# Optimization experiments

Hardware: AMD Instinct MI355X
Metric: run time of the kernel (lower is better)

The kernel has to match this reference:

```python
import jax, jax.numpy as jnp
import numpy as np

DIM = 96
WS = 16            # window_size
OVERLAP = 0.5
UPSCALE = 2
NH = 1             # num_heads
OWIN = int(WS * OVERLAP) + WS          # 24, overlap_win_size
WSU = UPSCALE * WS                     # 32, window_size_up
TABLE = (WSU + OWIN - 1) ** 2          # 3025
PAD = (OWIN - WS) // 2                 # 4


def compute_rpi():
    # Faithful to calculate_rpi_owxra (incl. torch negative-index wraparound -> modulo).
    wsu, cur = WSU, WS + int(OVERLAP * WS)
    a = np.arange(wsu)
    coords_up = np.stack(np.meshgrid(a, a, indexing='ij')).reshape(2, -1)      # (2, wsu^2)
    b = np.arange(cur)
    coords_cur = np.stack(np.meshgrid(b, b, indexing='ij')).reshape(2, -1)     # (2, cur^2)
    rel = coords_cur[:, None, :] - coords_up[:, :, None]                       # (2, wsu^2, cur^2)
    rel = rel.transpose(1, 2, 0).astype(np.int64)
    rel += wsu - cur + 1
    rel[:, :, 0] *= wsu + cur - 1
    idx = rel.sum(-1) % TABLE                                                  # (wsu^2, cur^2)
    return jnp.asarray(idx)


def setup_inputs() -> dict:
    key = jax.random.key(0)
    ks = jax.random.split(key, 6)
    x = jax.random.normal(ks[0], (2, 128, 128, DIM), dtype=jnp.float32)
    x2 = jax.random.normal(ks[1], (128, WSU * WSU, DIM), dtype=jnp.float32)  # (b*nw, 1024, 96)
    Wkv = jax.random.normal(ks[2], (DIM, 2 * DIM), dtype=jnp.float32) * 0.02
    bkv = jnp.zeros((2 * DIM,), dtype=jnp.float32)
    bias_table = jax.random.normal(ks[3], (TABLE, NH), dtype=jnp.float32) * 0.02
    Wproj = jax.random.normal(ks[4], (DIM, DIM), dtype=jnp.float32) * 0.02
    bproj = jnp.zeros((DIM,), dtype=jnp.float32)
    return {"x": x, "x2": x2, "Wkv": Wkv, "bkv": bkv,
            "bias_table": bias_table, "Wproj": Wproj, "bproj": bproj}


def _forward(x, x2, Wkv, bkv, bias_table, Wproj, bproj, rpi):
    b, h, w, c = x.shape
    d = c // NH
    scale = d ** (-0.5)
    kv = x @ Wkv + bkv                                        # (b,h,w,2c); cols [:c]=k, [c:]=v
    p = jnp.pad(kv, ((0, 0), (PAD, PAD), (PAD, PAD), (0, 0)))
    nwh, nww = h // WS, w // WS
    idx_h = (jnp.arange(nwh) * WS)[:, None] + jnp.arange(OWIN)  # (nwh, OWIN)
    idx_w = (jnp.arange(nww) * WS)[:, None] + jnp.arange(OWIN)
    rows = p[:, idx_h]                                        # (b,nwh,OWIN,W',2c)
    wins = rows[:, :, :, idx_w]                               # (b,nwh,OWIN,nww,OWIN,2c)
    wins = wins.transpose(0, 1, 3, 2, 4, 5).reshape(b * nwh * nww, OWIN * OWIN, 2 * c)
    k = wins[..., :c]
    v = wins[..., c:]
    nwb, Q, _ = x2.shape
    K = OWIN * OWIN
    q = x2.reshape(nwb, Q, NH, d).transpose(0, 2, 1, 3) * scale   # (nwb,nh,Q,d)
    kh = k.reshape(nwb, K, NH, d).transpose(0, 2, 1, 3)
    vh = v.reshape(nwb, K, NH, d).transpose(0, 2, 1, 3)
    attn = jnp.einsum('bhqd,bhkd->bhqk', q, kh)
    bias = bias_table[rpi].transpose(2, 0, 1)                  # (nh,Q,K)
    attn = jax.nn.softmax(attn + bias[None], axis=-1)
    out = jnp.einsum('bhqk,bhkd->bhqd', attn, vh)
    out = out.transpose(0, 2, 1, 3).reshape(nwb, Q, c)
    return out @ Wproj + bproj


def reference(x, x2, Wkv, bkv, bias_table, Wproj, bproj):
    rpi = compute_rpi()
    return _forward(x, x2, Wkv, bkv, bias_table, Wproj, bproj, rpi)
```

## Files before the change

kernel.cpp:

```cpp
#include <hip/hip_runtime.h>
#include <hip/hip_bf16.h>
#include <stdint.h>

#define QLEN 1024
#define KLEN 576
#define TABLE_SZ 3025

typedef __attribute__((ext_vector_type(8))) short short8;
typedef __attribute__((ext_vector_type(4))) float floatx4;
typedef __attribute__((ext_vector_type(4))) unsigned short ushort4v;

static __device__ __forceinline__ unsigned short f2b(float f) {
    union { float f; unsigned int u; } v; v.f = f;
    return (unsigned short)((v.u + 0x7FFFu + ((v.u >> 16) & 1u)) >> 16);
}
static __device__ __forceinline__ int pk2(float lo, float hi) {
    union { __hip_bfloat162 h; int i; } u;
    u.h = __float22bfloat162_rn(float2{lo, hi});
    return u.i;
}
union W8 { unsigned int u[4]; short8 s8; };

static __device__ __forceinline__ short8 redist(int A, int B, int C, int D, bool up, bool godd) {
    int Asw = __shfl_xor(A, 32), Bsw = __shfl_xor(B, 32);
    int Csw = __shfl_xor(C, 32), Dsw = __shfl_xor(D, 32);
    int E  = up ? Csw : A;
    int F  = up ? C   : Asw;
    int Eb = up ? Dsw : B;
    int Fb = up ? D   : Bsw;
    int E16 = __shfl_xor(E, 16), F16 = __shfl_xor(F, 16);
    int Eb16 = __shfl_xor(Eb, 16), Fb16 = __shfl_xor(Fb, 16);
    W8 w;
    w.u[0] = godd ? (unsigned)F16  : (unsigned)E;
    w.u[1] = godd ? (unsigned)Fb16 : (unsigned)Eb;
    w.u[2] = godd ? (unsigned)F    : (unsigned)E16;
    w.u[3] = godd ? (unsigned)Fb   : (unsigned)Eb16;
    return w.s8;
}

__global__ void prep_kernel(const float* __restrict__ Wkv, const float* __restrict__ Wproj,
                            const float* __restrict__ table,
                            unsigned short* __restrict__ WkvT, unsigned short* __restrict__ WprojT,
                            float* __restrict__ biasM) {
    const float LOG2E = 1.4426950408889634f;
    int t0 = blockIdx.x * blockDim.x + threadIdx.x;
    int stride = gridDim.x * blockDim.x;
    for (int i = t0; i < QLEN * KLEN; i += stride) {
        int qi = i / KLEN, kk = i - qi * KLEN;
        int rel0 = kk / 24 - qi / 32 + 9;
        int rel1 = kk % 24 - qi % 32 + 9;
        int s = rel0 * 55 + rel1;
        if (s < 0) s += TABLE_SZ;
        biasM[i] = table[s] * LOG2E;
    }
    for (int i = t0; i < 192 * 96; i += stride) {
        int n = i / 96, k = i - n * 96;
        WkvT[i] = f2b(Wkv[k * 192 + n]);
    }
    for (int i = t0; i < 96 * 96; i += stride) {
        int j = i / 96, d = i - j * 96;
        WprojT[i] = f2b(Wproj[d * 96 + j]);
    }
}

__global__ __launch_bounds__(256) void kv_kernel(const float* __restrict__ x,
        const unsigned short* __restrict__ WkvT, const float* __restrict__ bkv,
        unsigned short* __restrict__ Kpad, unsigned short* __restrict__ Vpad) {
    __shared__ unsigned short xt[64 * 104];
    __shared__ unsigned short vt2[96 * 72];
    int tid = threadIdx.x;
    int mbase = blockIdx.x * 64;
    int bb = mbase >> 14, rem = mbase & 16383;
    int hy = rem >> 7, hx0 = rem & 127;
    #pragma unroll
    for (int it = 0; it < 6; ++it) {
        int c = tid + it * 256;
        int row = c / 24, col4 = (c - row * 24) * 4;
        floatx4 v = *(const floatx4*)(x + (mbase + row) * 96 + col4);
        ushort4v o;
        o[0] = f2b(v[0]); o[1] = f2b(v[1]); o[2] = f2b(v[2]); o[3] = f2b(v[3]);
        *(ushort4v*)&xt[row * 104 + col4] = o;
    }
    __syncthreads();
    int lane = tid & 63, wv = tid >> 6;
    int g = lane >> 4, c16 = lane & 15;
    short8 a[3];
    #pragma unroll
    for (int c = 0; c < 3; ++c)
        a[c] = *(const short8*)&xt[(wv * 16 + c16) * 104 + c * 32 + g * 8];
    floatx4 acc[12];
    #pragma unroll
    for (int nt = 0; nt < 12; ++nt) acc[nt] = (floatx4){0.f, 0.f, 0.f, 0.f};
    #pragma unroll
    for (int nt = 0; nt < 12; ++nt)
        #pragma unroll
        for (int c = 0; c < 3; ++c) {
            short8 b = *(const short8*)(WkvT + (nt * 16 + c16) * 96 + c * 32 + g * 8);
            acc[nt] = __builtin_amdgcn_mfma_f32_16x16x32_bf16(a[c], b, acc[nt], 0, 0, 0);
        }
    #pragma unroll
    for (int nt = 0; nt < 6; ++nt) {
        int col = nt * 16 + c16;
        float bk = bkv[col];
        #pragma unroll
        for (int r = 0; r < 4; ++r) {
            int rowl = wv * 16 + g * 4 + r;
            Kpad[((bb * 136 + hy + 4) * 136 + hx0 + rowl + 4) * 96 + col] = f2b(acc[nt][r] + bk);
        }
    }
    #pragma unroll
    for (int nt = 6; nt < 12; ++nt) {
        int d = nt * 16 + c16 - 96;
        float bk = bkv[96 + d];
        #pragma unroll
        for (int r = 0; r < 4; ++r) {
            int rowl = wv * 16 + g * 4 + r;
            vt2[d * 72 + rowl] = f2b(acc[nt][r] + bk);
        }
    }
    __syncthreads();
    #pragma unroll
    for (int it = 0; it < 3; ++it) {
        int v = tid + it * 256;
        int d = v >> 3, ch = v & 7;
        short8 val = *(const short8*)&vt2[d * 72 + ch * 8];
        *(short8*)(Vpad + ((bb * 96 + d) * 136 + hy + 4) * 136 + hx0 + 4 + ch * 8) = val;
    }
}

__global__ __launch_bounds__(512, 4) void attn_kernel(const float* __restrict__ x2,
        const unsigned short* __restrict__ Kpad, const unsigned short* __restrict__ Vpad,
        const float* __restrict__ biasM,
        const unsigned short* __restrict__ WprojT, const float* __restrict__ bproj,
        float* __restrict__ out) {
    __shared__ unsigned short Kt[64 * 104];
    __shared__ unsigned short Vt[96 * 72];

    int bid_hw = blockIdx.x;
    int bid = (bid_hw & 7) * 128 + (bid_hw >> 3);
    int wb = bid >> 3, qb = bid & 7;
    int bb = wb >> 6, wy = (wb >> 3) & 7, wx = wb & 7;
    int tid = threadIdx.x, lane = tid & 63, wv = tid >> 6;
    int g = lane >> 4, c16 = lane & 15;
    int qlo = qb * 128 + wv * 16;
    bool up = (lane & 32) != 0;
    bool godd = (lane & 16) != 0;

    const float qscale = 0.10206207261596577f * 1.4426950408889634f;
    short8 qf[3];
    #pragma unroll
    for (int c = 0; c < 3; ++c) {
        const float* src = x2 + (wb * 1024 + qlo + c16) * 96 + c * 32 + g * 8;
        floatx4 v0 = *(const floatx4*)src;
        floatx4 v1 = *(const floatx4*)(src + 4);
        short8 q;
        #pragma unroll
        for (int i = 0; i < 4; ++i) {
            q[i]     = (short)f2b(v0[i] * qscale);
            q[4 + i] = (short)f2b(v1[i] * qscale);
        }
        qf[c] = q;
    }

    short8 pre[3];
    auto loadpre = [&](int kt) {
        #pragma unroll
        for (int it = 0; it < 3; ++it) {
            int c = tid + it * 512;
            if (c < 768) {
                int kr = c / 12, part = c - kr * 12;
                int kk = kt * 64 + kr;
                int oh = kk / 24, ow = kk - oh * 24;
                pre[it] = *(const short8*)(Kpad + ((bb * 136 + wy * 16 + oh) * 136 + wx * 16 + ow) * 96 + part * 8);
            } else {
                int v = c - 768;
                int d = v >> 3, ch = v & 7;
                int kk0 = kt * 64 + ch * 8;
                int oh = kk0 / 24, ow0 = kk0 - oh * 24;
                pre[it] = *(const short8*)(Vpad + ((bb * 96 + d) * 136 + wy * 16 + oh) * 136 + wx * 16 + ow0);
            }
        }
    };

    floatx4 Oa[6];
    #pragma unroll
    for (int dt = 0; dt < 6; ++dt) Oa[dt] = (floatx4){0.f, 0.f, 0.f, 0.f};
    float mrun = -1e30f, lrun = 0.f;

    loadpre(0);
    for (int kt = 0; kt < 9; ++kt) {
        __syncthreads();
        #pragma unroll
        for (int it = 0; it < 3; ++it) {
            int c = tid + it * 512;
            if (c < 768) {
                int kr = c / 12, part = c - kr * 12;
                *(short8*)&Kt[kr * 104 + part * 8] = pre[it];
            } else {
                int v = c - 768;
                int d = v >> 3, ch = v & 7;
                *(short8*)&Vt[d * 72 + ch * 8] = pre[it];
            }
        }
        if (kt < 8) loadpre(kt + 1);
        __syncthreads();

        float sv[4][4];
        __builtin_amdgcn_s_setprio(1);
        #pragma unroll
        for (int sub = 0; sub < 4; ++sub) {
            floatx4 acc = (floatx4){0.f, 0.f, 0.f, 0.f};
            #pragma unroll
            for (int c = 0; c < 3; ++c) {
                short8 kf = *(const short8*)&Kt[(sub * 16 + c16) * 104 + c * 32 + g * 8];
                acc = __builtin_amdgcn_mfma_f32_16x16x32_bf16(kf, qf[c], acc, 0, 0, 0);
            }
            floatx4 bv = *(const floatx4*)(biasM + (qlo + c16) * 576 + kt * 64 + sub * 16 + g * 4);
            #pragma unroll
            for (int r = 0; r < 4; ++r) sv[sub][r] = acc[r] + bv[r];
        }
        __builtin_amdgcn_s_setprio(0);

        float tm = sv[0][0];
        #pragma unroll
        for (int sub = 0; sub < 4; ++sub)
            #pragma unroll
            for (int r = 0; r < 4; ++r) tm = fmaxf(tm, sv[sub][r]);
        tm = fmaxf(tm, __shfl_xor(tm, 16));
        tm = fmaxf(tm, __shfl_xor(tm, 32));
        if (!__all(tm <= mrun + 8.f)) {
            float mn = fmaxf(mrun, tm);
            float fac = __builtin_amdgcn_exp2f(mrun - mn);
            mrun = mn;
            lrun *= fac;
            #pragma unroll
            for (int dt = 0; dt < 6; ++dt)
                #pragma unroll
                for (int r = 0; r < 4; ++r) Oa[dt][r] *= fac;
        }
        float ts = 0.f;
        #pragma unroll
        for (int sub = 0; sub < 4; ++sub)
            #pragma unroll
            for (int r = 0; r < 4; ++r) {
                float p = __builtin_amdgcn_exp2f(sv[sub][r] - mrun);
                sv[sub][r] = p;
                ts += p;
            }
        ts += __shfl_xor(ts, 16);
        ts += __shfl_xor(ts, 32);
        lrun += ts;

        #pragma unroll
        for (int kc = 0; kc < 2; ++kc) {
            int A = pk2(sv[2 * kc][0], sv[2 * kc][1]);
            int B = pk2(sv[2 * kc][2], sv[2 * kc][3]);
            int C = pk2(sv[2 * kc + 1][0], sv[2 * kc + 1][1]);
            int D = pk2(sv[2 * kc + 1][2], sv[2 * kc + 1][3]);
            short8 pf = redist(A, B, C, D, up, godd);
            __builtin_amdgcn_s_setprio(1);
            #pragma unroll
            for (int dt = 0; dt < 6; ++dt) {
                short8 vf = *(const short8*)&Vt[(dt * 16 + c16) * 72 + kc * 32 + g * 8];
                Oa[dt] = __builtin_amdgcn_mfma_f32_16x16x32_bf16(vf, pf, Oa[dt], 0, 0, 0);
            }
            __builtin_amdgcn_s_setprio(0);
        }
    }

    float inv = 1.0f / lrun;
    int w2[6][2];
    #pragma unroll
    for (int dt = 0; dt < 6; ++dt) {
        w2[dt][0] = pk2(Oa[dt][0] * inv, Oa[dt][1] * inv);
        w2[dt][1] = pk2(Oa[dt][2] * inv, Oa[dt][3] * inv);
    }
    short8 of[3];
    #pragma unroll
    for (int kc = 0; kc < 3; ++kc)
        of[kc] = redist(w2[2 * kc][0], w2[2 * kc][1], w2[2 * kc + 1][0], w2[2 * kc + 1][1], up, godd);
    #pragma unroll
    for (int jt = 0; jt < 6; ++jt) {
        floatx4 acc = (floatx4){0.f, 0.f, 0.f, 0.f};
        #pragma unroll
        for (int kc = 0; kc < 3; ++kc) {
            short8 wf = *(const short8*)(WprojT + (jt * 16 + c16) * 96 + kc * 32 + g * 8);
            acc = __builtin_amdgcn_mfma_f32_16x16x32_bf16(of[kc], wf, acc, 0, 0, 0);
        }
        int col = jt * 16 + c16;
        float bp = bproj[col];
        #pragma unroll
        for (int r = 0; r < 4; ++r)
            out[(wb * 1024 + qlo + g * 4 + r) * 96 + col] = acc[r] + bp;
    }
}

extern "C" void kernel_launch(void* const* d_in, const int* in_sizes, int n_in,
                              void* d_out, int out_size, void* d_ws, size_t ws_size,
                              hipStream_t stream) {
    const float* x     = (const float*)d_in[0];
    const float* x2    = (const float*)d_in[1];
    const float* Wkv   = (const float*)d_in[2];
    const float* bkv   = (const float*)d_in[3];
    const float* table = (const float*)d_in[4];
    const float* Wproj = (const float*)d_in[5];
    const float* bproj = (const float*)d_in[6];
    float* out = (float*)d_out;

    char* ws = (char*)d_ws;
    unsigned short* Kpad   = (unsigned short*)ws;
    unsigned short* Vpad   = (unsigned short*)(ws + 7102464);
    float*          biasM  = (float*)(ws + 14204928);
    unsigned short* WkvT   = (unsigned short*)(ws + 16564224);
    unsigned short* WprojT = (unsigned short*)(ws + 16601088);

    hipMemsetAsync(ws, 0, 14204928, stream);
    hipLaunchKernelGGL(prep_kernel, dim3(512), dim3(256), 0, stream,
                       Wkv, Wproj, table, WkvT, WprojT, biasM);
    hipLaunchKernelGGL(kv_kernel, dim3(512), dim3(256), 0, stream,
                       x, WkvT, bkv, Kpad, Vpad);
    hipLaunchKernelGGL(attn_kernel, dim3(1024), dim3(512), 0, stream,
                       x2, Kpad, Vpad, biasM, WprojT, bproj, out);
}
```

Before: 107.2 us.

## Process two query tiles per wave and double-buffer K/V shared tiles

Each wave now handles 32 query rows as two 16-row sub-tiles, so every K and V fragment read from shared memory feeds two MFMAs. The block shrinks to 256 threads and the K/V tiles in shared memory are double-buffered, which removes one of the two barriers per key tile. The cost is roughly doubled accumulator and score registers per wave and twice the shared memory per block, which may lower occupancy and give fewer waves to hide latency.

```diff
diff --git a/kernel.cpp b/kernel.cpp
--- a/kernel.cpp
+++ b/kernel.cpp
@@ -128,13 +128,13 @@
     }
 }
 
-__global__ __launch_bounds__(512, 4) void attn_kernel(const float* __restrict__ x2,
+__global__ __launch_bounds__(256, 3) void attn_kernel(const float* __restrict__ x2,
         const unsigned short* __restrict__ Kpad, const unsigned short* __restrict__ Vpad,
         const float* __restrict__ biasM,
         const unsigned short* __restrict__ WprojT, const float* __restrict__ bproj,
         float* __restrict__ out) {
-    __shared__ unsigned short Kt[64 * 104];
-    __shared__ unsigned short Vt[96 * 72];
+    __shared__ unsigned short Kt[2][64 * 104];
+    __shared__ unsigned short Vt[2][96 * 72];
 
     int bid_hw = blockIdx.x;
     int bid = (bid_hw & 7) * 128 + (bid_hw >> 3);
@@ -142,31 +142,33 @@
     int bb = wb >> 6, wy = (wb >> 3) & 7, wx = wb & 7;
     int tid = threadIdx.x, lane = tid & 63, wv = tid >> 6;
     int g = lane >> 4, c16 = lane & 15;
-    int qlo = qb * 128 + wv * 16;
+    int qlo = qb * 128 + wv * 32;
     bool up = (lane & 32) != 0;
     bool godd = (lane & 16) != 0;
 
     const float qscale = 0.10206207261596577f * 1.4426950408889634f;
-    short8 qf[3];
-    #pragma unroll
-    for (int c = 0; c < 3; ++c) {
-        const float* src = x2 + (wb * 1024 + qlo + c16) * 96 + c * 32 + g * 8;
-        floatx4 v0 = *(const floatx4*)src;
-        floatx4 v1 = *(const floatx4*)(src + 4);
-        short8 q;
-        #pragma unroll
-        for (int i = 0; i < 4; ++i) {
-            q[i]     = (short)f2b(v0[i] * qscale);
-            q[4 + i] = (short)f2b(v1[i] * qscale);
-        }
-        qf[c] = q;
-    }
-
-    short8 pre[3];
+    short8 qf[2][3];
+    #pragma unroll
+    for (int s = 0; s < 2; ++s)
+        #pragma unroll
+        for (int c = 0; c < 3; ++c) {
+            const float* src = x2 + (wb * 1024 + qlo + s * 16 + c16) * 96 + c * 32 + g * 8;
+            floatx4 v0 = *(const floatx4*)src;
+            floatx4 v1 = *(const floatx4*)(src + 4);
+            short8 q;
+            #pragma unroll
+            for (int i = 0; i < 4; ++i) {
+                q[i]     = (short)f2b(v0[i] * qscale);
+                q[4 + i] = (short)f2b(v1[i] * qscale);
+            }
+            qf[s][c] = q;
+        }
+
+    short8 pre[6];
     auto loadpre = [&](int kt) {
         #pragma unroll
-        for (int it = 0; it < 3; ++it) {
-            int c = tid + it * 512;
+        for (int it = 0; it < 6; ++it) {
+            int c = tid + it * 256;
             if (c < 768) {
                 int kr = c / 12, part = c - kr * 12;
                 int kk = kt * 64 + kr;
@@ -181,117 +183,152 @@
             }
         }
     };
-
-    floatx4 Oa[6];
-    #pragma unroll
-    for (int dt = 0; dt < 6; ++dt) Oa[dt] = (floatx4){0.f, 0.f, 0.f, 0.f};
-    float mrun = -1e30f, lrun = 0.f;
-
-    loadpre(0);
-    for (int kt = 0; kt < 9; ++kt) {
-        __syncthreads();
-        #pragma unroll
-        for (int it = 0; it < 3; ++it) {
-            int c = tid + it * 512;
+    auto store_buf = [&](int b) {
+        #pragma unroll
+        for (int it = 0; it < 6; ++it) {
+            int c = tid + it * 256;
             if (c < 768) {
                 int kr = c / 12, part = c - kr * 12;
-                *(short8*)&Kt[kr * 104 + part * 8] = pre[it];
+                *(short8*)&Kt[b][kr * 104 + part * 8] = pre[it];
             } else {
                 int v = c - 768;
                 int d = v >> 3, ch = v & 7;
-                *(short8*)&Vt[d * 72 + ch * 8] = pre[it];
-            }
-        }
-        if (kt < 8) loadpre(kt + 1);
+                *(short8*)&Vt[b][d * 72 + ch * 8] = pre[it];
+            }
+        }
+    };
+
+    floatx4 Oa[2][6];
+    #pragma unroll
+    for (int s = 0; s < 2; ++s)
+        #pragma unroll
+        for (int dt = 0; dt < 6; ++dt) Oa[s][dt] = (floatx4){0.f, 0.f, 0.f, 0.f};
+    float mrun[2] = {-1e30f, -1e30f}, lrun[2] = {0.f, 0.f};
+
+    loadpre(0);
+    store_buf(0);
+    loadpre(1);
+    __syncthreads();
+
+    for (int kt = 0; kt < 9; ++kt) {
+        int cur = kt & 1;
+        if (kt < 8) {
+            store_buf(cur ^ 1);
+            if (kt < 7) loadpre(kt + 2);
+        }
+
+        float sv[2][4][4];
+        __builtin_amdgcn_s_setprio(1);
+        #pragma unroll
+        for (int sub = 0; sub < 4; ++sub) {
+            floatx4 a0 = (floatx4){0.f, 0.f, 0.f, 0.f};
+            floatx4 a1 = (floatx4){0.f, 0.f, 0.f, 0.f};
+            #pragma unroll
+            for (int c = 0; c < 3; ++c) {
+                short8 kf = *(const short8*)&Kt[cur][(sub * 16 + c16) * 104 + c * 32 + g * 8];
+                a0 = __builtin_amdgcn_mfma_f32_16x16x32_bf16(kf, qf[0][c], a0, 0, 0, 0);
+                a1 = __builtin_amdgcn_mfma_f32_16x16x32_bf16(kf, qf[1][c], a1, 0, 0, 0);
+            }
+            floatx4 bv0 = *(const floatx4*)(biasM + (qlo + c16) * 576 + kt * 64 + sub * 16 + g * 4);
+            floatx4 bv1 = *(const floatx4*)(biasM + (qlo + 16 + c16) * 576 + kt * 64 + sub * 16 + g * 4);
+            #pragma unroll
+            for (int r = 0; r < 4; ++r) { sv[0][sub][r] = a0[r] + bv0[r]; sv[1][sub][r] = a1[r] + bv1[r]; }
+        }
+        __builtin_amdgcn_s_setprio(0);
+
+        #pragma unroll
+        for (int s = 0; s < 2; ++s) {
+            float tm = sv[s][0][0];
+            #pragma unroll
+            for (int sub = 0; sub < 4; ++sub)
+                #pragma unroll
+                for (int r = 0; r < 4; ++r) tm = fmaxf(tm, sv[s][sub][r]);
+            tm = fmaxf(tm, __shfl_xor(tm, 16));
+            tm = fmaxf(tm, __shfl_xor(tm, 32));
+            if (!__all(tm <= mrun[s] + 8.f)) {
+                float mn = fmaxf(mrun[s], tm);
+                float fac = __builtin_amdgcn_exp2f(mrun[s] - mn);
+                mrun[s] = mn;
+                lrun[s] *= fac;
+                #pragma unroll
+                for (int dt = 0; dt < 6; ++dt)
+                    #pragma unroll
+                    for (int r = 0; r < 4; ++r) Oa[s][dt][r] *= fac;
+            }
+            float ts = 0.f;
+            #pragma unroll
+            for (int sub = 0; sub < 4; ++sub)
+                #pragma unroll
+                for (int r = 0; r < 4; ++r) {
+                    float p = __builtin_amdgcn_exp2f(sv[s][sub][r] - mrun[s]);
+                    sv[s][sub][r] = p;
+                    ts += p;
+                }
+            ts += __shfl_xor(ts, 16);
+            ts += __shfl_xor(ts, 32);
+            lrun[s] += ts;
+        }
+
+        #pragma unroll
+        for (int kc = 0; kc < 2; ++kc) {
+            short8 pf0, pf1;
+            {
+                int A = pk2(sv[0][2 * kc][0], sv[0][2 * kc][1]);
+                int B = pk2(sv[0][2 * kc][2], sv[0][2 * kc][3]);
+                int C = pk2(sv[0][2 * kc + 1][0], sv[0][2 * kc + 1][1]);
+                int D = pk2(sv[0][2 * kc + 1][2], sv[0][2 * kc + 1][3]);
+                pf0 = redist(A, B, C, D, up, godd);
+            }
+            {
+                int A = pk2(sv[1][2 * kc][0], sv[1][2 * kc][1]);
+                int B = pk2(sv[1][2 * kc][2], sv[1][2 * kc][3]);
+                int C = pk2(sv[1][2 * kc + 1][0], sv[1][2 * kc + 1][1]);
+                int D = pk2(sv[1][2 * kc + 1][2], sv[1][2 * kc + 1][3]);
+                pf1 = redist(A, B, C, D, up, godd);
+            }
+            __builtin_amdgcn_s_setprio(1);
+            #pragma unroll
+            for (int dt = 0; dt < 6; ++dt) {
+                short8 vf = *(const short8*)&Vt[cur][(dt * 16 + c16) * 72 + kc * 32 + g * 8];
+                Oa[0][dt] = __builtin_amdgcn_mfma_f32_16x16x32_bf16(vf, pf0, Oa[0][dt], 0, 0, 0);
+                Oa[1][dt] = __builtin_amdgcn_mfma_f32_16x16x32_bf16(vf, pf1, Oa[1][dt], 0, 0, 0);
+            }
+            __builtin_amdgcn_s_setprio(0);
+        }
         __syncthreads();
-
-        float sv[4][4];
-        __builtin_amdgcn_s_setprio(1);
-        #pragma unroll
-        for (int sub = 0; sub < 4; ++sub) {
-            floatx4 acc = (floatx4){0.f, 0.f, 0.f, 0.f};
-            #pragma unroll
-            for (int c = 0; c < 3; ++c) {
-                short8 kf = *(const short8*)&Kt[(sub * 16 + c16) * 104 + c * 32 + g * 8];
-                acc = __builtin_amdgcn_mfma_f32_16x16x32_bf16(kf, qf[c], acc, 0, 0, 0);
-            }
-            floatx4 bv = *(const floatx4*)(biasM + (qlo + c16) * 576 + kt * 64 + sub * 16 + g * 4);
-            #pragma unroll
-            for (int r = 0; r < 4; ++r) sv[sub][r] = acc[r] + bv[r];
-        }
-        __builtin_amdgcn_s_setprio(0);
-
-        float tm = sv[0][0];
-        #pragma unroll
-        for (int sub = 0; sub < 4; ++sub)
-            #pragma unroll
-            for (int r = 0; r < 4; ++r) tm = fmaxf(tm, sv[sub][r]);
-        tm = fmaxf(tm, __shfl_xor(tm, 16));
-        tm = fmaxf(tm, __shfl_xor(tm, 32));
-        if (!__all(tm <= mrun + 8.f)) {
-            float mn = fmaxf(mrun, tm);
-            float fac = __builtin_amdgcn_exp2f(mrun - mn);
-            mrun = mn;
-            lrun *= fac;
-            #pragma unroll
-            for (int dt = 0; dt < 6; ++dt)
-                #pragma unroll
-                for (int r = 0; r < 4; ++r) Oa[dt][r] *= fac;
-        }
-        float ts = 0.f;
-        #pragma unroll
-        for (int sub = 0; sub < 4; ++sub)
-            #pragma unroll
-            for (int r = 0; r < 4; ++r) {
-                float p = __builtin_amdgcn_exp2f(sv[sub][r] - mrun);
-                sv[sub][r] = p;
-                ts += p;
-            }
-        ts += __shfl_xor(ts, 16);
-        ts += __shfl_xor(ts, 32);
-        lrun += ts;
-
-        #pragma unroll
-        for (int kc = 0; kc < 2; ++kc) {
-            int A = pk2(sv[2 * kc][0], sv[2 * kc][1]);
-            int B = pk2(sv[2 * kc][2], sv[2 * kc][3]);
-            int C = pk2(sv[2 * kc + 1][0], sv[2 * kc + 1][1]);
-            int D = pk2(sv[2 * kc + 1][2], sv[2 * kc + 1][3]);
-            short8 pf = redist(A, B, C, D, up, godd);
-            __builtin_amdgcn_s_setprio(1);
-            #pragma unroll
-            for (int dt = 0; dt < 6; ++dt) {
-                short8 vf = *(const short8*)&Vt[(dt * 16 + c16) * 72 + kc * 32 + g * 8];
-                Oa[dt] = __builtin_amdgcn_mfma_f32_16x16x32_bf16(vf, pf, Oa[dt], 0, 0, 0);
-            }
-            __builtin_amdgcn_s_setprio(0);
-        }
-    }
-
-    float inv = 1.0f / lrun;
-    int w2[6][2];
-    #pragma unroll
-    for (int dt = 0; dt < 6; ++dt) {
-        w2[dt][0] = pk2(Oa[dt][0] * inv, Oa[dt][1] * inv);
-        w2[dt][1] = pk2(Oa[dt][2] * inv, Oa[dt][3] * inv);
-    }
-    short8 of[3];
-    #pragma unroll
-    for (int kc = 0; kc < 3; ++kc)
-        of[kc] = redist(w2[2 * kc][0], w2[2 * kc][1], w2[2 * kc + 1][0], w2[2 * kc + 1][1], up, godd);
+    }
+
+    short8 of[2][3];
+    #pragma unroll
+    for (int s = 0; s < 2; ++s) {
+        float inv = 1.0f / lrun[s];
+        int w2[6][2];
+        #pragma unroll
+        for (int dt = 0; dt < 6; ++dt) {
+            w2[dt][0] = pk2(Oa[s][dt][0] * inv, Oa[s][dt][1] * inv);
+            w2[dt][1] = pk2(Oa[s][dt][2] * inv, Oa[s][dt][3] * inv);
+        }
+        #pragma unroll
+        for (int kc = 0; kc < 3; ++kc)
+            of[s][kc] = redist(w2[2 * kc][0], w2[2 * kc][1], w2[2 * kc + 1][0], w2[2 * kc + 1][1], up, godd);
+    }
     #pragma unroll
     for (int jt = 0; jt < 6; ++jt) {
-        floatx4 acc = (floatx4){0.f, 0.f, 0.f, 0.f};
+        floatx4 acc0 = (floatx4){0.f, 0.f, 0.f, 0.f};
+        floatx4 acc1 = (floatx4){0.f, 0.f, 0.f, 0.f};
         #pragma unroll
         for (int kc = 0; kc < 3; ++kc) {
             short8 wf = *(const short8*)(WprojT + (jt * 16 + c16) * 96 + kc * 32 + g * 8);
-            acc = __builtin_amdgcn_mfma_f32_16x16x32_bf16(of[kc], wf, acc, 0, 0, 0);
+            acc0 = __builtin_amdgcn_mfma_f32_16x16x32_bf16(of[0][kc], wf, acc0, 0, 0, 0);
+            acc1 = __builtin_amdgcn_mfma_f32_16x16x32_bf16(of[1][kc], wf, acc1, 0, 0, 0);
         }
         int col = jt * 16 + c16;
         float bp = bproj[col];
         #pragma unroll
-        for (int r = 0; r < 4; ++r)
-            out[(wb * 1024 + qlo + g * 4 + r) * 96 + col] = acc[r] + bp;
+        for (int r = 0; r < 4; ++r) {
+            out[(wb * 1024 + qlo + g * 4 + r) * 96 + col]      = acc0[r] + bp;
+            out[(wb * 1024 + qlo + 16 + g * 4 + r) * 96 + col] = acc1[r] + bp;
+        }
     }
 }
 
@@ -319,6 +356,6 @@
                        Wkv, Wproj, table, WkvT, WprojT, biasM);
     hipLaunchKernelGGL(kv_kernel, dim3(512), dim3(256), 0, stream,
                        x, WkvT, bkv, Kpad, Vpad);
-    hipLaunchKernelGGL(attn_kernel, dim3(1024), dim3(512), 0, stream,
+    hipLaunchKernelGGL(attn_kernel, dim3(1024), dim3(256), 0, stream,
                        x2, Kpad, Vpad, biasM, WprojT, bproj, out);
 }
```

New measurement: 164.4 us. 1.53x slower.
